# Kernel optimization log

Hardware: AMD Instinct MI355X
Metric: run time of the kernel (lower is better)

Reference implementation:

```python
import jax, jax.numpy as jnp
import numpy as np

N_SRC = 100000
N_DST = 100000
E = 1600000
D_IN = 64
D_OUT = 64
LN_EPS = 1e-5


def setup_inputs() -> dict:
    key = jax.random.key(0)
    k1, k2, k3, k4, k5 = jax.random.split(key, 5)
    feat = jax.random.normal(k1, (N_SRC, D_IN), dtype=jnp.float32)
    edge_src = jax.random.randint(k2, (E,), 0, N_SRC, dtype=jnp.int32)
    edge_dst = jax.random.randint(k3, (E,), 0, N_DST, dtype=jnp.int32)
    W_w = jax.random.normal(k4, (D_IN, D_OUT), dtype=jnp.float32) * (1.0 / np.sqrt(D_IN))
    film_w = jax.random.normal(k5, (D_IN, 2 * D_OUT), dtype=jnp.float32) * (1.0 / np.sqrt(D_IN))
    ln_scale = jnp.ones((D_OUT,), dtype=jnp.float32)
    ln_bias = jnp.zeros((D_OUT,), dtype=jnp.float32)
    return {"feat": feat, "edge_src": edge_src, "edge_dst": edge_dst,
            "W_w": W_w, "film_w": film_w, "ln_scale": ln_scale, "ln_bias": ln_bias}


def reference(feat, edge_src, edge_dst, W_w, film_w, ln_scale, ln_bias):
    # messages = relu(gamma * (feat @ W) + beta), gamma/beta from film linear
    msg = feat @ W_w                                  # [N_src, D_OUT]
    film = feat @ film_w                              # [N_src, 2*D_OUT]
    gamma, beta = film[:, :D_OUT], film[:, D_OUT:]
    msg = jax.nn.relu(gamma * msg + beta)             # [N_src, D_OUT]
    # copy_u + sum: scatter-sum messages from source nodes to destinations
    h = jax.ops.segment_sum(msg[edge_src], edge_dst, num_segments=N_DST)  # [N_dst, D_OUT]
    # LayerNorm over feature dim (dropout is identity in eval)
    mu = jnp.mean(h, axis=-1, keepdims=True)
    var = jnp.var(h, axis=-1, keepdims=True)
    out = (h - mu) * jax.lax.rsqrt(var + LN_EPS) * ln_scale + ln_bias
    return out
```

## Files before the change

kernel.cpp:

```cpp
#include <hip/hip_runtime.h>

constexpr int N_SRC = 100000;
constexpr int N_DST = 100000;
constexpr int E     = 1600000;
constexpr int D     = 64;
constexpr float LN_EPS = 1e-5f;

constexpr int NCHUNK = 512;
constexpr int CHUNK  = E / NCHUNK;
constexpr int BROWS  = 128;
constexpr int NBK    = (N_DST + BROWS - 1) / BROWS;
constexpr int MAXB   = 4096;

typedef __attribute__((ext_vector_type(8))) short bf16x8;
typedef __attribute__((ext_vector_type(4))) float f32x4;

__device__ inline unsigned short bfh(float x) {
    union { float f; unsigned u; } c; c.f = x; return (unsigned short)(c.u >> 16);
}
__device__ inline float bff(unsigned short b) {
    union { unsigned u; float f; } c; c.u = (unsigned)b << 16; return c.f;
}
__device__ inline float asf(unsigned u) {
    union { unsigned u; float f; } c; c.u = u; return c.f;
}
__device__ inline unsigned short bfrne(float x) {
    union { float f; unsigned u; } c; c.f = x;
    unsigned u = c.u + (0x7FFFu + ((c.u >> 16) & 1u));
    return (unsigned short)(u >> 16);
}

__global__ __launch_bounds__(256) void k_film(const float* __restrict__ feat,
                                              const float* __restrict__ Ww,
                                              const float* __restrict__ Fw,
                                              unsigned short* __restrict__ msgb) {
    const int lane = threadIdx.x & 63;
    const int wid  = threadIdx.x >> 6;
    const int w    = blockIdx.x * 4 + wid;
    const int m    = lane & 15;
    const int kg   = lane >> 4;
    const int mrow0 = w * 64;

    bf16x8 ahi[4][2], alo[4][2];
#pragma unroll
    for (int mt = 0; mt < 4; ++mt) {
        const int rbase = mrow0 + mt * 16 + m;
        const int r = (rbase < N_SRC) ? rbase : 0;
#pragma unroll
        for (int ks = 0; ks < 2; ++ks) {
            const float* p = feat + (size_t)r * 64 + ks * 32 + kg * 8;
            const float4 x0 = *reinterpret_cast<const float4*>(p);
            const float4 x1 = *reinterpret_cast<const float4*>(p + 4);
            const float a[8] = {x0.x, x0.y, x0.z, x0.w, x1.x, x1.y, x1.z, x1.w};
            bf16x8 h, l;
#pragma unroll
            for (int j = 0; j < 8; ++j) {
                const unsigned short hb = bfh(a[j]);
                h[j] = (short)hb;
                l[j] = (short)bfh(a[j] - bff(hb));
            }
            ahi[mt][ks] = h; alo[mt][ks] = l;
        }
    }

    const f32x4 zero = {0.f, 0.f, 0.f, 0.f};

#pragma unroll
    for (int t = 0; t < 4; ++t) {
        f32x4 am[4], ag[4], ab[4];
#pragma unroll
        for (int i = 0; i < 4; ++i) { am[i] = zero; ag[i] = zero; ab[i] = zero; }

#pragma unroll
        for (int ks = 0; ks < 2; ++ks) {
            bf16x8 wmh, wml, wgh, wgl, wbh, wbl;
#pragma unroll
            for (int j = 0; j < 8; ++j) {
                const int k = ks * 32 + kg * 8 + j;
                const int n = t * 16 + m;
                const float vm = Ww[k * 64 + n];
                const float vg = Fw[k * 128 + n];
                const float vb = Fw[k * 128 + 64 + n];
                unsigned short hb;
                hb = bfh(vm); wmh[j] = (short)hb; wml[j] = (short)bfh(vm - bff(hb));
                hb = bfh(vg); wgh[j] = (short)hb; wgl[j] = (short)bfh(vg - bff(hb));
                hb = bfh(vb); wbh[j] = (short)hb; wbl[j] = (short)bfh(vb - bff(hb));
            }
#pragma unroll
            for (int mt = 0; mt < 4; ++mt) {
                am[mt] = __builtin_amdgcn_mfma_f32_16x16x32_bf16(ahi[mt][ks], wmh, am[mt], 0, 0, 0);
                am[mt] = __builtin_amdgcn_mfma_f32_16x16x32_bf16(ahi[mt][ks], wml, am[mt], 0, 0, 0);
                am[mt] = __builtin_amdgcn_mfma_f32_16x16x32_bf16(alo[mt][ks], wmh, am[mt], 0, 0, 0);
                ag[mt] = __builtin_amdgcn_mfma_f32_16x16x32_bf16(ahi[mt][ks], wgh, ag[mt], 0, 0, 0);
                ag[mt] = __builtin_amdgcn_mfma_f32_16x16x32_bf16(ahi[mt][ks], wgl, ag[mt], 0, 0, 0);
                ag[mt] = __builtin_amdgcn_mfma_f32_16x16x32_bf16(alo[mt][ks], wgh, ag[mt], 0, 0, 0);
                ab[mt] = __builtin_amdgcn_mfma_f32_16x16x32_bf16(ahi[mt][ks], wbh, ab[mt], 0, 0, 0);
                ab[mt] = __builtin_amdgcn_mfma_f32_16x16x32_bf16(ahi[mt][ks], wbl, ab[mt], 0, 0, 0);
                ab[mt] = __builtin_amdgcn_mfma_f32_16x16x32_bf16(alo[mt][ks], wbh, ab[mt], 0, 0, 0);
            }
        }

#pragma unroll
        for (int mt = 0; mt < 4; ++mt) {
            const int rb = mrow0 + mt * 16;
            if (rb < N_SRC) {
#pragma unroll
                for (int r4 = 0; r4 < 4; ++r4) {
                    const int row = rb + kg * 4 + r4;
                    const float o = fmaxf(ag[mt][r4] * am[mt][r4] + ab[mt][r4], 0.f);
                    msgb[(size_t)row * 64 + t * 16 + m] = bfrne(o);
                }
            }
        }
    }
}

__global__ __launch_bounds__(256) void k_hist1(const int* __restrict__ edst,
                                               int* __restrict__ H) {
    __shared__ int hl[NBK];
    for (int i = threadIdx.x; i < NBK; i += 256) hl[i] = 0;
    __syncthreads();
    const int c = blockIdx.x;
    const int e0 = c * CHUNK;
    for (int e = e0 + threadIdx.x; e < e0 + CHUNK; e += 256)
        atomicAdd(&hl[edst[e] >> 7], 1);
    __syncthreads();
    for (int i = threadIdx.x; i < NBK; i += 256) H[i * NCHUNK + c] = hl[i];
}

__global__ __launch_bounds__(512) void k_scanH(int* __restrict__ H,
                                               int* __restrict__ bstart) {
    const int k = blockIdx.x;
    const int c = threadIdx.x;
    const int lane = c & 63;
    const int wid = c >> 6;
    const int v = H[k * NCHUNK + c];
    int x = v;
#pragma unroll
    for (int o = 1; o < 64; o <<= 1) { int y = __shfl_up(x, o); if (lane >= o) x += y; }
    __shared__ int wsum[8];
    if (lane == 63) wsum[wid] = x;
    __syncthreads();
    int add = 0;
    for (int w = 0; w < wid; ++w) add += wsum[w];
    const int incl = x + add;
    H[k * NCHUNK + c] = incl - v;
    if (c == NCHUNK - 1) bstart[k] = incl;
}

__global__ __launch_bounds__(64) void k_h3(int* __restrict__ bstart) {
    const int lane = threadIdx.x;
    int running = 0;
    for (int b = 0; b < NBK; b += 64) {
        const int idx = b + lane;
        const int v = (idx < NBK) ? bstart[idx] : 0;
        int x = v;
#pragma unroll
        for (int o = 1; o < 64; o <<= 1) { int y = __shfl_up(x, o); if (lane >= o) x += y; }
        if (idx < NBK) bstart[idx] = running + x - v;
        running += __shfl(x, 63);
    }
    if (lane == 0) bstart[NBK] = E;
}

__global__ __launch_bounds__(256) void k_pairs(const int* __restrict__ esrc,
                                               const int* __restrict__ edst,
                                               const int* __restrict__ H,
                                               const int* __restrict__ bstart,
                                               unsigned* __restrict__ pairs) {
    __shared__ int curs[NBK];
    const int c = blockIdx.x;
    for (int i = threadIdx.x; i < NBK; i += 256) curs[i] = bstart[i] + H[i * NCHUNK + c];
    __syncthreads();
    const int e0 = c * CHUNK;
    for (int e = e0 + threadIdx.x; e < e0 + CHUNK; e += 256) {
        const int d = edst[e];
        const int s = esrc[e];
        const int k = d >> 7;
        const int pos = atomicAdd(&curs[k], 1);
        pairs[pos] = ((unsigned)(d & 127) << 24) | (unsigned)s;
    }
}

__global__ __launch_bounds__(256) void k_reduce2(const unsigned short* __restrict__ msgb,
                                                 const unsigned* __restrict__ pairs,
                                                 const int* __restrict__ bstart,
                                                 const float* __restrict__ sc,
                                                 const float* __restrict__ bi,
                                                 float* __restrict__ out) {
    __shared__ int srcs[MAXB];
    __shared__ int cnt[BROWS];
    __shared__ int off[BROWS];
    __shared__ int cur[BROWS];

    const int k = blockIdx.x;
    const int tid = threadIdx.x;
    const int lane = tid & 63;
    const int wid = tid >> 6;
    const int s0 = bstart[k];
    const int s1 = bstart[k + 1];

    for (int i = tid; i < BROWS; i += 256) cnt[i] = 0;
    __syncthreads();

    for (int i = s0 + tid; i < s1; i += 256) atomicAdd(&cnt[pairs[i] >> 24], 1);
    __syncthreads();

    if (tid < 64) {
        const int a = cnt[lane];
        const int b = cnt[64 + lane];
        int xa = a, xb = b;
#pragma unroll
        for (int o = 1; o < 64; o <<= 1) {
            int ya = __shfl_up(xa, o); if (lane >= o) xa += ya;
            int yb = __shfl_up(xb, o); if (lane >= o) xb += yb;
        }
        const int tot_a = __shfl(xa, 63);
        off[lane]      = xa - a;
        off[64 + lane] = tot_a + xb - b;
        cur[lane]      = off[lane];
        cur[64 + lane] = off[64 + lane];
    }
    __syncthreads();

    for (int i = s0 + tid; i < s1; i += 256) {
        const unsigned p = pairs[i];
        const int pos = atomicAdd(&cur[p >> 24], 1);
        if (pos < MAXB) srcs[pos] = (int)(p & 0x1FFFFu);
    }
    __syncthreads();

    const int q = lane >> 4;
    const int c = lane & 15;

    for (int r = wid; r < BROWS; r += 4) {
        const int dst = k * BROWS + r;
        if (dst >= N_DST) break;
        const int rn = cnt[r];
        const int ro = off[r];

        float ax = 0.f, ay = 0.f, az = 0.f, aw = 0.f;
        for (int b0 = 0; b0 < rn; b0 += 32) {
            int sj[8]; bool okv[8];
#pragma unroll
            for (int j = 0; j < 8; ++j) {
                const int ei = b0 + 4 * j + q;
                okv[j] = ei < rn;
                sj[j] = srcs[ro + min(ei, rn - 1)];
            }
#pragma unroll
            for (int j = 0; j < 8; ++j) {
                if (b0 + 4 * j >= rn) break;
                const uint2 v = *reinterpret_cast<const uint2*>(
                    msgb + (size_t)sj[j] * D + c * 4);
                const unsigned msk = okv[j] ? 0xFFFFFFFFu : 0u;
                const unsigned vx = v.x & msk, vy = v.y & msk;
                ax += asf(vx << 16);
                ay += asf(vx & 0xFFFF0000u);
                az += asf(vy << 16);
                aw += asf(vy & 0xFFFF0000u);
            }
        }

        ax += __shfl_xor(ax, 32); ay += __shfl_xor(ay, 32);
        az += __shfl_xor(az, 32); aw += __shfl_xor(aw, 32);
        ax += __shfl_xor(ax, 16); ay += __shfl_xor(ay, 16);
        az += __shfl_xor(az, 16); aw += __shfl_xor(aw, 16);

        float s = (ax + ay) + (az + aw);
#pragma unroll
        for (int o = 8; o > 0; o >>= 1) s += __shfl_xor(s, o);
        const float mu = s * (1.0f / D);
        const float dx = ax - mu, dy = ay - mu, dz = az - mu, dw = aw - mu;
        float s2 = (dx * dx + dy * dy) + (dz * dz + dw * dw);
#pragma unroll
        for (int o = 8; o > 0; o >>= 1) s2 += __shfl_xor(s2, o);
        const float rs = rsqrtf(s2 * (1.0f / D) + LN_EPS);

        if (lane < 16) {
            const float4 scv = *reinterpret_cast<const float4*>(sc + c * 4);
            const float4 biv = *reinterpret_cast<const float4*>(bi + c * 4);
            float4 o4;
            o4.x = dx * rs * scv.x + biv.x;
            o4.y = dy * rs * scv.y + biv.y;
            o4.z = dz * rs * scv.z + biv.z;
            o4.w = dw * rs * scv.w + biv.w;
            *reinterpret_cast<float4*>(out + (size_t)dst * D + c * 4) = o4;
        }
    }
}

extern "C" void kernel_launch(void* const* d_in, const int* in_sizes, int n_in,
                              void* d_out, int out_size, void* d_ws, size_t ws_size,
                              hipStream_t stream) {
    const float* feat = (const float*)d_in[0];
    const int*   esrc = (const int*)d_in[1];
    const int*   edst = (const int*)d_in[2];
    const float* Ww   = (const float*)d_in[3];
    const float* Fw   = (const float*)d_in[4];
    const float* sc   = (const float*)d_in[5];
    const float* bi   = (const float*)d_in[6];
    float* out = (float*)d_out;

    char* ws = (char*)d_ws;
    unsigned short* msgb = (unsigned short*)(ws);
    unsigned* pairs  = (unsigned*)(ws + 26u * 1024 * 1024);
    int*      H      = (int*)(ws + 33u * 1024 * 1024);
    int*      bstart = (int*)(ws + 35u * 1024 * 1024);

    k_film  <<<391, 256, 0, stream>>>(feat, Ww, Fw, msgb);
    k_hist1 <<<NCHUNK, 256, 0, stream>>>(edst, H);
    k_scanH <<<NBK, 512, 0, stream>>>(H, bstart);
    k_h3    <<<1, 64, 0, stream>>>(bstart);
    k_pairs <<<NCHUNK, 256, 0, stream>>>(esrc, edst, H, bstart, pairs);
    k_reduce2<<<NBK, 256, 0, stream>>>(msgb, pairs, bstart, sc, bi, out);
}
```

Measured before the change: 232.8 us.

## Stage split-bf16 weights in LDS for FiLM, halve rows per wave, widen reduce blocks

k_film now converts the three weight matrices into hi/lo bf16 halves once per block and stores them in padded shared memory. Each wave then reads its weight fragments from LDS instead of repeating strided global loads and conversions per wave. Rows per wave drop from 64 to 32 and the grid doubles to raise parallelism. k_reduce2 goes from 256 to 512 threads per block, so eight waves share the destination rows, at the cost of more threads contending on the shared-memory atomics.

```diff
diff --git a/kernel.cpp b/kernel.cpp
--- a/kernel.cpp
+++ b/kernel.cpp
@@ -11,6 +11,7 @@
 constexpr int BROWS  = 128;
 constexpr int NBK    = (N_DST + BROWS - 1) / BROWS;
 constexpr int MAXB   = 4096;
+constexpr int FB     = 72;
 
 typedef __attribute__((ext_vector_type(8))) short bf16x8;
 typedef __attribute__((ext_vector_type(4))) float f32x4;
@@ -34,16 +35,18 @@
                                               const float* __restrict__ Ww,
                                               const float* __restrict__ Fw,
                                               unsigned short* __restrict__ msgb) {
-    const int lane = threadIdx.x & 63;
-    const int wid  = threadIdx.x >> 6;
-    const int w    = blockIdx.x * 4 + wid;
+    __shared__ unsigned short wl[6 * 64 * FB];
+
+    const int tid  = threadIdx.x;
+    const int lane = tid & 63;
+    const int wid  = tid >> 6;
     const int m    = lane & 15;
     const int kg   = lane >> 4;
-    const int mrow0 = w * 64;
-
-    bf16x8 ahi[4][2], alo[4][2];
-#pragma unroll
-    for (int mt = 0; mt < 4; ++mt) {
+    const int mrow0 = (blockIdx.x * 4 + wid) * 32;
+
+    bf16x8 ahi[2][2], alo[2][2];
+#pragma unroll
+    for (int mt = 0; mt < 2; ++mt) {
         const int rbase = mrow0 + mt * 16 + m;
         const int r = (rbase < N_SRC) ? rbase : 0;
 #pragma unroll
@@ -63,31 +66,49 @@
         }
     }
 
+    for (int task = tid; task < 1536; task += 256) {
+        const int g  = task & 7;
+        const int n  = (task >> 3) & 63;
+        const int mu = task >> 9;
+        const float* src;
+        int stride;
+        if (mu == 0)      { src = Ww + n;       stride = 64;  }
+        else if (mu == 1) { src = Fw + n;       stride = 128; }
+        else              { src = Fw + 64 + n;  stride = 128; }
+        bf16x8 h, l;
+#pragma unroll
+        for (int j = 0; j < 8; ++j) {
+            const float v = src[(size_t)(8 * g + j) * stride];
+            const unsigned short hb = bfh(v);
+            h[j] = (short)hb;
+            l[j] = (short)bfh(v - bff(hb));
+        }
+        *reinterpret_cast<bf16x8*>(&wl[(2 * mu + 0) * 64 * FB + n * FB + g * 8]) = h;
+        *reinterpret_cast<bf16x8*>(&wl[(2 * mu + 1) * 64 * FB + n * FB + g * 8]) = l;
+    }
+    __syncthreads();
+
     const f32x4 zero = {0.f, 0.f, 0.f, 0.f};
 
 #pragma unroll
     for (int t = 0; t < 4; ++t) {
-        f32x4 am[4], ag[4], ab[4];
-#pragma unroll
-        for (int i = 0; i < 4; ++i) { am[i] = zero; ag[i] = zero; ab[i] = zero; }
+        f32x4 am[2], ag[2], ab[2];
+#pragma unroll
+        for (int i = 0; i < 2; ++i) { am[i] = zero; ag[i] = zero; ab[i] = zero; }
 
 #pragma unroll
         for (int ks = 0; ks < 2; ++ks) {
-            bf16x8 wmh, wml, wgh, wgl, wbh, wbl;
-#pragma unroll
-            for (int j = 0; j < 8; ++j) {
-                const int k = ks * 32 + kg * 8 + j;
-                const int n = t * 16 + m;
-                const float vm = Ww[k * 64 + n];
-                const float vg = Fw[k * 128 + n];
-                const float vb = Fw[k * 128 + 64 + n];
-                unsigned short hb;
-                hb = bfh(vm); wmh[j] = (short)hb; wml[j] = (short)bfh(vm - bff(hb));
-                hb = bfh(vg); wgh[j] = (short)hb; wgl[j] = (short)bfh(vg - bff(hb));
-                hb = bfh(vb); wbh[j] = (short)hb; wbl[j] = (short)bfh(vb - bff(hb));
-            }
-#pragma unroll
-            for (int mt = 0; mt < 4; ++mt) {
+            const int n = t * 16 + m;
+            const int koff = ks * 32 + kg * 8;
+            const int base = n * FB + koff;
+            const bf16x8 wmh = *reinterpret_cast<const bf16x8*>(&wl[0 * 64 * FB + base]);
+            const bf16x8 wml = *reinterpret_cast<const bf16x8*>(&wl[1 * 64 * FB + base]);
+            const bf16x8 wgh = *reinterpret_cast<const bf16x8*>(&wl[2 * 64 * FB + base]);
+            const bf16x8 wgl = *reinterpret_cast<const bf16x8*>(&wl[3 * 64 * FB + base]);
+            const bf16x8 wbh = *reinterpret_cast<const bf16x8*>(&wl[4 * 64 * FB + base]);
+            const bf16x8 wbl = *reinterpret_cast<const bf16x8*>(&wl[5 * 64 * FB + base]);
+#pragma unroll
+            for (int mt = 0; mt < 2; ++mt) {
                 am[mt] = __builtin_amdgcn_mfma_f32_16x16x32_bf16(ahi[mt][ks], wmh, am[mt], 0, 0, 0);
                 am[mt] = __builtin_amdgcn_mfma_f32_16x16x32_bf16(ahi[mt][ks], wml, am[mt], 0, 0, 0);
                 am[mt] = __builtin_amdgcn_mfma_f32_16x16x32_bf16(alo[mt][ks], wmh, am[mt], 0, 0, 0);
@@ -101,7 +122,7 @@
         }
 
 #pragma unroll
-        for (int mt = 0; mt < 4; ++mt) {
+        for (int mt = 0; mt < 2; ++mt) {
             const int rb = mrow0 + mt * 16;
             if (rb < N_SRC) {
 #pragma unroll
@@ -182,7 +203,7 @@
     }
 }
 
-__global__ __launch_bounds__(256) void k_reduce2(const unsigned short* __restrict__ msgb,
+__global__ __launch_bounds__(512) void k_reduce2(const unsigned short* __restrict__ msgb,
                                                  const unsigned* __restrict__ pairs,
                                                  const int* __restrict__ bstart,
                                                  const float* __restrict__ sc,
@@ -200,10 +221,10 @@
     const int s0 = bstart[k];
     const int s1 = bstart[k + 1];
 
-    for (int i = tid; i < BROWS; i += 256) cnt[i] = 0;
-    __syncthreads();
-
-    for (int i = s0 + tid; i < s1; i += 256) atomicAdd(&cnt[pairs[i] >> 24], 1);
+    for (int i = tid; i < BROWS; i += 512) cnt[i] = 0;
+    __syncthreads();
+
+    for (int i = s0 + tid; i < s1; i += 512) atomicAdd(&cnt[pairs[i] >> 24], 1);
     __syncthreads();
 
     if (tid < 64) {
@@ -223,7 +244,7 @@
     }
     __syncthreads();
 
-    for (int i = s0 + tid; i < s1; i += 256) {
+    for (int i = s0 + tid; i < s1; i += 512) {
         const unsigned p = pairs[i];
         const int pos = atomicAdd(&cur[p >> 24], 1);
         if (pos < MAXB) srcs[pos] = (int)(p & 0x1FFFFu);
@@ -233,7 +254,7 @@
     const int q = lane >> 4;
     const int c = lane & 15;
 
-    for (int r = wid; r < BROWS; r += 4) {
+    for (int r = wid; r < BROWS; r += 8) {
         const int dst = k * BROWS + r;
         if (dst >= N_DST) break;
         const int rn = cnt[r];
@@ -308,10 +329,10 @@
     int*      H      = (int*)(ws + 33u * 1024 * 1024);
     int*      bstart = (int*)(ws + 35u * 1024 * 1024);
 
-    k_film  <<<391, 256, 0, stream>>>(feat, Ww, Fw, msgb);
+    k_film  <<<782, 256, 0, stream>>>(feat, Ww, Fw, msgb);
     k_hist1 <<<NCHUNK, 256, 0, stream>>>(edst, H);
     k_scanH <<<NBK, 512, 0, stream>>>(H, bstart);
     k_h3    <<<1, 64, 0, stream>>>(bstart);
     k_pairs <<<NCHUNK, 256, 0, stream>>>(esrc, edst, H, bstart, pairs);
-    k_reduce2<<<NBK, 256, 0, stream>>>(msgb, pairs, bstart, sc, bi, out);
-}
+    k_reduce2<<<NBK, 512, 0, stream>>>(msgb, pairs, bstart, sc, bi, out);
+}
```

Result: faster. 205.6 us (-11.7%).
